# Optimization experiments

Measured on AMD Instinct MI355X. Metric: run time of the kernel, lower is better.

Reference implementation:

```python
import jax, jax.numpy as jnp
import numpy as np

DIM = 1024
N_HEAD = 16
HEAD_DIM = DIM // N_HEAD
B, T = 2, 2048


def setup_inputs() -> dict:
    key = jax.random.key(0)
    ks = jax.random.split(key, 9)
    s = 1.0 / np.sqrt(DIM)
    return {
        "x": jax.random.normal(ks[0], (B, T, DIM), dtype=jnp.float32),
        "Wq": jax.random.normal(ks[1], (DIM, DIM), dtype=jnp.float32) * s,
        "bq": jax.random.normal(ks[2], (DIM,), dtype=jnp.float32) * s,
        "Wk": jax.random.normal(ks[3], (DIM, DIM), dtype=jnp.float32) * s,
        "bk": jax.random.normal(ks[4], (DIM,), dtype=jnp.float32) * s,
        "Wv": jax.random.normal(ks[5], (DIM, DIM), dtype=jnp.float32) * s,
        "bv": jax.random.normal(ks[6], (DIM,), dtype=jnp.float32) * s,
        "Wo": jax.random.normal(ks[7], (DIM, DIM), dtype=jnp.float32) * s,
        "bo": jax.random.normal(ks[8], (DIM,), dtype=jnp.float32) * s,
    }


def reference(x, Wq, bq, Wk, bk, Wv, bv, Wo, bo):
    b, t, d = x.shape
    # torch nn.Linear: y = x @ W.T + b
    Q = x @ Wq.T + bq  # [b, t, d]
    K = x @ Wk.T + bk
    V = x @ Wv.T + bv
    # split heads -> [b, h, t, hd]
    Q = Q.reshape(b, t, N_HEAD, HEAD_DIM).transpose(0, 2, 1, 3)
    K = K.reshape(b, t, N_HEAD, HEAD_DIM).transpose(0, 2, 1, 3)
    V = V.reshape(b, t, N_HEAD, HEAD_DIM).transpose(0, 2, 1, 3)
    scale = 1.0 / jnp.sqrt(jnp.float32(HEAD_DIM))
    score = jnp.einsum('bhqd,bhkd->bhqk', Q, K) * scale  # [b, h, t, t]
    attn = jax.nn.softmax(score, axis=-1)
    # dropout is identity in eval mode
    out = jnp.einsum('bhqk,bhkd->bhqd', attn, V)  # [b, h, t, hd]
    out = out.transpose(0, 2, 1, 3).reshape(b, t, d)
    return out @ Wo.T + bo
```

## Files before the change

### kernel.cpp

```cpp
#include <hip/hip_runtime.h>


#define DIM 1024
#define NH 16
#define HD 64
#define SEQ 2048
#define NROWS 4096

typedef unsigned short u16;
typedef unsigned int u32;
typedef __bf16 bf16_t;
typedef bf16_t bf16x8 __attribute__((ext_vector_type(8)));
typedef float f32x4 __attribute__((ext_vector_type(4)));
typedef u16 u16x4 __attribute__((ext_vector_type(4)));
typedef short i16x4 __attribute__((ext_vector_type(4)));
typedef u32 u32x2 __attribute__((ext_vector_type(2)));

typedef const __attribute__((address_space(1))) void* gas_ptr;
typedef __attribute__((address_space(3))) void* las_ptr;

#define S_BARRIER() asm volatile("s_barrier" ::: "memory")
#define S_WAITCNT_VM(N) asm volatile("s_waitcnt vmcnt(" #N ")" ::: "memory")

__device__ __forceinline__ void gl_lds16(const void* g, void* lds_wave_base) {
  __builtin_amdgcn_global_load_lds((gas_ptr)g, (las_ptr)lds_wave_base, 16, 0, 0);
}

__device__ __forceinline__ f32x4 mfma_bf16(bf16x8 a, bf16x8 b, f32x4 c) {
  return __builtin_amdgcn_mfma_f32_16x16x32_bf16(a, b, c, 0, 0, 0);
}

__device__ __forceinline__ f32x4 mfma16_bf16(i16x4 a, i16x4 b, f32x4 c) {
#if __has_builtin(__builtin_amdgcn_mfma_f32_16x16x16bf16_1k)
  return __builtin_amdgcn_mfma_f32_16x16x16bf16_1k(a, b, c, 0, 0, 0);
#else
  asm("v_mfma_f32_16x16x16_bf16 %0, %1, %2, %0" : "+v"(c) : "v"(a), "v"(b));
  return c;
#endif
}

__device__ __forceinline__ u32 cvtpk(float lo, float hi) {
  u32 r;
  asm("v_cvt_pk_bf16_f32 %0, %1, %2" : "=v"(r) : "v"(lo), "v"(hi));
  return r;
}

__device__ __forceinline__ u16 bfu(float f) {
  bf16_t b = (bf16_t)f;
  union { bf16_t b; u16 u; } cv; cv.b = b; return cv.u;
}

__device__ __forceinline__ float fexp2(float x) {
#if __has_builtin(__builtin_amdgcn_exp2f)
  return __builtin_amdgcn_exp2f(x);
#else
  return exp2f(x);
#endif
}

#define QSCALE 0.18033688f

__global__ void cvt_x(const float* __restrict__ in, u16* __restrict__ out) {
  int i = blockIdx.x * 256 + threadIdx.x;
  float4 v = ((const float4*)in)[i];
  u16x4 o;
  o.x = bfu(v.x); o.y = bfu(v.y); o.z = bfu(v.z); o.w = bfu(v.w);
  ((u16x4*)out)[i] = o;
}

__global__ void cvt_w4(const float* __restrict__ wq, const float* __restrict__ wk,
                       const float* __restrict__ wv, const float* __restrict__ wo,
                       u16* __restrict__ oq, u16* __restrict__ ok,
                       u16* __restrict__ ov, u16* __restrict__ oo) {
  const int which = blockIdx.y;
  const float* in = which == 0 ? wq : which == 1 ? wk : which == 2 ? wv : wo;
  u16* out = which == 0 ? oq : which == 1 ? ok : which == 2 ? ov : oo;
  const float s = which == 0 ? QSCALE : 1.0f;
  int i = blockIdx.x * 256 + threadIdx.x;
  float4 v = ((const float4*)in)[i];
  u16x4 o;
  o.x = bfu(v.x * s); o.y = bfu(v.y * s); o.z = bfu(v.z * s); o.w = bfu(v.w * s);
  ((u16x4*)out)[i] = o;
}

__device__ __forceinline__ int xcd_swz(int L, int nwg) {
  return (L & 7) * (nwg >> 3) + (L >> 3);
}

__global__ __launch_bounds__(256, 3) void gemm_qkv(const u16* __restrict__ A,
                                                   const u16* __restrict__ wq,
                                                   const u16* __restrict__ wk,
                                                   const u16* __restrict__ wv,
                                                   const float* __restrict__ bq,
                                                   const float* __restrict__ bk,
                                                   const float* __restrict__ bv,
                                                   u16* __restrict__ Qb,
                                                   u16* __restrict__ Kb,
                                                   u16* __restrict__ Vtb) {
  __shared__ u16 As[2][128 * 32];
  __shared__ u16 Bs[2][128 * 32];
  const int L = blockIdx.y * gridDim.x + blockIdx.x;
  const int swz = xcd_swz(L, gridDim.x * gridDim.y);
  const int bx = swz % gridDim.x, by = swz / gridDim.x;
  const int which = bx >> 3;
  const int col0 = (bx & 7) * 128;
  const u16* W = which == 0 ? wq : which == 1 ? wk : wv;
  const float* bias = which == 0 ? bq : which == 1 ? bk : bv;
  const float bscale = which == 0 ? QSCALE : 1.0f;

  const int t = threadIdx.x, lane = t & 63, w = t >> 6;
  const int row0 = by * 128;
  const int wr = w >> 1, wc = w & 1;
  const int lr = lane & 15, lk = lane >> 4;

  f32x4 acc[4][4] = {};

  auto stage = [&](int k0, int bu) {
#pragma unroll
    for (int i = 0; i < 2; ++i) {
      const int bc = i * 256 + w * 64;
      const int f = bc + lane;
      gl_lds16(A + (size_t)(row0 + (f >> 2)) * DIM + k0 + (f & 3) * 8, &As[bu][bc * 8]);
      gl_lds16(W + (size_t)(col0 + (f >> 2)) * DIM + k0 + (f & 3) * 8, &Bs[bu][bc * 8]);
    }
  };

  stage(0, 0);
  int buf = 0;
  for (int k0 = 0; k0 < DIM; k0 += 32) {
    if (k0 + 32 < DIM) { stage(k0 + 32, buf ^ 1); S_WAITCNT_VM(4); }
    else               { S_WAITCNT_VM(0); }
    S_BARRIER();

    bf16x8 a[4], b[4];
#pragma unroll
    for (int m = 0; m < 4; ++m)
      a[m] = *(const bf16x8*)&As[buf][(wr * 64 + m * 16 + lr) * 32 + lk * 8];
#pragma unroll
    for (int n = 0; n < 4; ++n)
      b[n] = *(const bf16x8*)&Bs[buf][(wc * 64 + n * 16 + lr) * 32 + lk * 8];
    __builtin_amdgcn_s_setprio(1);
#pragma unroll
    for (int m = 0; m < 4; ++m)
#pragma unroll
      for (int n = 0; n < 4; ++n)
        acc[m][n] = mfma_bf16(a[m], b[n], acc[m][n]);
    __builtin_amdgcn_s_setprio(0);

    S_BARRIER();
    buf ^= 1;
  }

#pragma unroll
  for (int m = 0; m < 4; ++m) {
    const int rowb = row0 + wr * 64 + m * 16 + lk * 4;
#pragma unroll
    for (int n = 0; n < 4; ++n) {
      const int ocol = col0 + wc * 64 + n * 16 + lr;
      const float bc = bias[ocol] * bscale;
#pragma unroll
      for (int r = 0; r < 4; ++r) {
        const int rr = rowb + r;
        const float v = acc[m][n][r] + bc;
        if (which == 0) {
          Qb[(size_t)rr * DIM + ocol] = bfu(v);
        } else if (which == 1) {
          Kb[(size_t)rr * DIM + ocol] = bfu(v);
        } else {
          const size_t idx = ((((size_t)(rr >> 11) * NH + (ocol >> 6)) * HD + (ocol & 63)) << 11) + (rr & 2047);
          Vtb[idx] = bfu(v);
        }
      }
    }
  }
}

__global__ __launch_bounds__(256, 3) void gemm_out(const u16* __restrict__ A,
                                                   const u16* __restrict__ W,
                                                   const float* __restrict__ bias,
                                                   float* __restrict__ C) {
  __shared__ u16 As[2][128 * 32];
  __shared__ u16 Bs[2][128 * 32];
  const int L = blockIdx.y * gridDim.x + blockIdx.x;
  const int swz = xcd_swz(L, gridDim.x * gridDim.y);
  const int bx = swz % gridDim.x, by = swz / gridDim.x;
  const int t = threadIdx.x, lane = t & 63, w = t >> 6;
  const int row0 = by * 128, col0 = bx * 128;
  const int wr = w >> 1, wc = w & 1;
  const int lr = lane & 15, lk = lane >> 4;

  f32x4 acc[4][4] = {};

  auto stage = [&](int k0, int bu) {
#pragma unroll
    for (int i = 0; i < 2; ++i) {
      const int bc = i * 256 + w * 64;
      const int f = bc + lane;
      gl_lds16(A + (size_t)(row0 + (f >> 2)) * DIM + k0 + (f & 3) * 8, &As[bu][bc * 8]);
      gl_lds16(W + (size_t)(col0 + (f >> 2)) * DIM + k0 + (f & 3) * 8, &Bs[bu][bc * 8]);
    }
  };

  stage(0, 0);
  int buf = 0;
  for (int k0 = 0; k0 < DIM; k0 += 32) {
    if (k0 + 32 < DIM) { stage(k0 + 32, buf ^ 1); S_WAITCNT_VM(4); }
    else               { S_WAITCNT_VM(0); }
    S_BARRIER();

    bf16x8 a[4], b[4];
#pragma unroll
    for (int m = 0; m < 4; ++m)
      a[m] = *(const bf16x8*)&As[buf][(wr * 64 + m * 16 + lr) * 32 + lk * 8];
#pragma unroll
    for (int n = 0; n < 4; ++n)
      b[n] = *(const bf16x8*)&Bs[buf][(wc * 64 + n * 16 + lr) * 32 + lk * 8];
    __builtin_amdgcn_s_setprio(1);
#pragma unroll
    for (int m = 0; m < 4; ++m)
#pragma unroll
      for (int n = 0; n < 4; ++n)
        acc[m][n] = mfma_bf16(a[m], b[n], acc[m][n]);
    __builtin_amdgcn_s_setprio(0);

    S_BARRIER();
    buf ^= 1;
  }

#pragma unroll
  for (int m = 0; m < 4; ++m) {
    const int rowb = row0 + wr * 64 + m * 16 + lk * 4;
#pragma unroll
    for (int n = 0; n < 4; ++n) {
      const int col = col0 + wc * 64 + n * 16 + lr;
      const float bc = bias[col];
#pragma unroll
      for (int r = 0; r < 4; ++r)
        C[(size_t)(rowb + r) * DIM + col] = acc[m][n][r] + bc;
    }
  }
}

__global__ __launch_bounds__(256, 5) void flash_attn(const u16* __restrict__ Q,
                                                     const u16* __restrict__ K,
                                                     const u16* __restrict__ Vt,
                                                     u16* __restrict__ O) {
  __shared__ u16 Ks[2][64 * 64];
  __shared__ u16 Vs[2][64 * 64];

  const int t = threadIdx.x, lane = t & 63, w = t >> 6;
  const int L = blockIdx.x;
  const int bh = ((L >> 8) << 3) | (L & 7);
  const int qt = (L >> 3) & 31;
  const int b = bh >> 4, h = bh & 15;
  const int q0 = qt * 64;
  const int lr = lane & 15, lk = lane >> 4;

  const size_t qrow = (size_t)(b * SEQ + q0 + w * 16 + lr);
  bf16x8 qf[2];
  qf[0] = *(const bf16x8*)&Q[qrow * DIM + h * HD + lk * 8];
  qf[1] = *(const bf16x8*)&Q[qrow * DIM + h * HD + lk * 8 + 32];

  f32x4 o[4] = {};
  float m0 = -INFINITY, l0 = 0.f;

  auto stage = [&](int kt, int bu) {
#pragma unroll
    for (int i = 0; i < 2; ++i) {
      const int bc = i * 256 + w * 64;
      const int f = bc + lane;
      const int row = f >> 3, c = f & 7;
      const int cs = c ^ (row & 7);
      gl_lds16(K + (size_t)(b * SEQ + kt + row) * DIM + h * HD + cs * 8, &Ks[bu][bc * 8]);
      gl_lds16(Vt + (((size_t)bh * HD + row) << 11) + kt + cs * 8, &Vs[bu][bc * 8]);
    }
  };

  stage(0, 0);
  int buf = 0;
  for (int kt = 0; kt < SEQ; kt += 64) {
    if (kt + 64 < SEQ) { stage(kt + 64, buf ^ 1); S_WAITCNT_VM(4); }
    else               { S_WAITCNT_VM(0); }
    S_BARRIER();

    const u16* ks = Ks[buf];
    const u16* vs = Vs[buf];

    f32x4 s[4] = {};
    __builtin_amdgcn_s_setprio(1);
#pragma unroll
    for (int n = 0; n < 4; ++n) {
      const int row = n * 16 + lr;
#pragma unroll
      for (int kk = 0; kk < 2; ++kk) {
        bf16x8 kf = *(const bf16x8*)&ks[row * 64 + (((lk + kk * 4) ^ (row & 7)) * 8)];
        s[n] = mfma_bf16(kf, qf[kk], s[n]);
      }
    }
    __builtin_amdgcn_s_setprio(0);

    f32x4 m4 = s[0];
#pragma unroll
    for (int n = 1; n < 4; ++n) {
      m4[0] = fmaxf(m4[0], s[n][0]); m4[1] = fmaxf(m4[1], s[n][1]);
      m4[2] = fmaxf(m4[2], s[n][2]); m4[3] = fmaxf(m4[3], s[n][3]);
    }
    float mx = fmaxf(fmaxf(m4[0], m4[1]), fmaxf(m4[2], m4[3]));
    mx = fmaxf(mx, __shfl_xor(mx, 16));
    mx = fmaxf(mx, __shfl_xor(mx, 32));
    if (__any(mx > m0 + 8.0f)) {
      const float mnew = fmaxf(m0, mx);
      const float alpha = fexp2(m0 - mnew);
      m0 = mnew;
      l0 *= alpha;
#pragma unroll
      for (int r = 0; r < 4; ++r) {
        const float a_r = __shfl(alpha, lk * 4 + r);
#pragma unroll
        for (int nd = 0; nd < 4; ++nd) o[nd][r] *= a_r;
      }
    }

    float p[4][4];
    float rs = 0.f;
#pragma unroll
    for (int n = 0; n < 4; ++n)
#pragma unroll
      for (int r = 0; r < 4; ++r) { p[n][r] = fexp2(s[n][r] - m0); rs += p[n][r]; }
    rs += __shfl_xor(rs, 16);
    rs += __shfl_xor(rs, 32);
    l0 += rs;

    i16x4 paf[4];
#pragma unroll
    for (int n = 0; n < 4; ++n) {
      u32x2 pk;
      pk[0] = cvtpk(p[n][0], p[n][1]);
      pk[1] = cvtpk(p[n][2], p[n][3]);
      paf[n] = __builtin_bit_cast(i16x4, pk);
    }

    __builtin_amdgcn_s_setprio(1);
#pragma unroll
    for (int n = 0; n < 4; ++n) {
#pragma unroll
      for (int nd = 0; nd < 4; ++nd) {
        const int vrow = nd * 16 + lr;
        const int chunk = (2 * n + (lk >> 1)) ^ (vrow & 7);
        i16x4 vb = *(const i16x4*)&vs[vrow * 64 + chunk * 8 + (lk & 1) * 4];
        o[nd] = mfma16_bf16(paf[n], vb, o[nd]);
      }
    }
    __builtin_amdgcn_s_setprio(0);

    S_BARRIER();
    buf ^= 1;
  }

#pragma unroll
  for (int r = 0; r < 4; ++r) {
    const float inv = 1.f / __shfl(l0, lk * 4 + r);
    const size_t grow = (size_t)(b * SEQ + q0 + w * 16 + lk * 4 + r);
#pragma unroll
    for (int nd = 0; nd < 4; ++nd)
      O[grow * DIM + h * HD + nd * 16 + lr] = bfu(o[nd][r] * inv);
  }
}

extern "C" void kernel_launch(void* const* d_in, const int* in_sizes, int n_in,
                              void* d_out, int out_size, void* d_ws, size_t ws_size,
                              hipStream_t stream) {
  (void)in_sizes; (void)n_in; (void)out_size; (void)ws_size;
  const float* x  = (const float*)d_in[0];
  const float* Wq = (const float*)d_in[1];
  const float* bq = (const float*)d_in[2];
  const float* Wk = (const float*)d_in[3];
  const float* bk = (const float*)d_in[4];
  const float* Wv = (const float*)d_in[5];
  const float* bv = (const float*)d_in[6];
  const float* Wo = (const float*)d_in[7];
  const float* bo = (const float*)d_in[8];

  char* ws = (char*)d_ws;
  u16* xb  = (u16*)(ws + 0);
  u16* wqb = (u16*)(ws + 8388608);
  u16* wkb = (u16*)(ws + 10485760);
  u16* wvb = (u16*)(ws + 12582912);
  u16* wob = (u16*)(ws + 14680064);
  u16* Qb  = (u16*)(ws + 16777216);
  u16* Kb  = (u16*)(ws + 25165824);
  u16* Vtb = (u16*)(ws + 33554432);
  u16* Ob  = (u16*)(ws + 41943040);

  cvt_x<<<NROWS * DIM / 4 / 256, 256, 0, stream>>>(x, xb);
  cvt_w4<<<dim3(DIM * DIM / 4 / 256, 4), 256, 0, stream>>>(Wq, Wk, Wv, Wo, wqb, wkb, wvb, wob);

  gemm_qkv<<<dim3(24, NROWS / 128), 256, 0, stream>>>(xb, wqb, wkb, wvb, bq, bk, bv, Qb, Kb, Vtb);

  flash_attn<<<1024, 256, 0, stream>>>(Qb, Kb, Vtb, Ob);

  gemm_out<<<dim3(DIM / 128, NROWS / 128), 256, 0, stream>>>(Ob, wob, bo, (float*)d_out);
}
```

Baseline: 139.5 us.

## Split attention over two KV halves with a combine kernel and LDS-staged P

Splits each query tile's key range into two halves processed by separate blocks, doubling the grid and raising occupancy (launch bounds 8). Each block writes unnormalized partial outputs plus running max and sum, and a new combine kernel merges them with log-sum-exp rescaling. The KV tile shrinks to 32, and probabilities are staged through LDS so PV uses the wider 16x16x32 MFMA. This adds an extra kernel launch and extra global traffic for the partial results.

```diff
diff --git a/kernel.cpp b/kernel.cpp
--- a/kernel.cpp
+++ b/kernel.cpp
@@ -13,7 +13,6 @@
 typedef bf16_t bf16x8 __attribute__((ext_vector_type(8)));
 typedef float f32x4 __attribute__((ext_vector_type(4)));
 typedef u16 u16x4 __attribute__((ext_vector_type(4)));
-typedef short i16x4 __attribute__((ext_vector_type(4)));
 typedef u32 u32x2 __attribute__((ext_vector_type(2)));
 
 typedef const __attribute__((address_space(1))) void* gas_ptr;
@@ -28,15 +27,6 @@
 
 __device__ __forceinline__ f32x4 mfma_bf16(bf16x8 a, bf16x8 b, f32x4 c) {
   return __builtin_amdgcn_mfma_f32_16x16x32_bf16(a, b, c, 0, 0, 0);
-}
-
-__device__ __forceinline__ f32x4 mfma16_bf16(i16x4 a, i16x4 b, f32x4 c) {
-#if __has_builtin(__builtin_amdgcn_mfma_f32_16x16x16bf16_1k)
-  return __builtin_amdgcn_mfma_f32_16x16x16bf16_1k(a, b, c, 0, 0, 0);
-#else
-  asm("v_mfma_f32_16x16x16_bf16 %0, %1, %2, %0" : "+v"(c) : "v"(a), "v"(b));
-  return c;
-#endif
 }
 
 __device__ __forceinline__ u32 cvtpk(float lo, float hi) {
@@ -48,6 +38,10 @@
 __device__ __forceinline__ u16 bfu(float f) {
   bf16_t b = (bf16_t)f;
   union { bf16_t b; u16 u; } cv; cv.b = b; return cv.u;
+}
+
+__device__ __forceinline__ float b2f(u16 u) {
+  union { u32 u; float f; } cv; cv.u = ((u32)u) << 16; return cv.f;
 }
 
 __device__ __forceinline__ float fexp2(float x) {
@@ -241,17 +235,22 @@
   }
 }
 
-__global__ __launch_bounds__(256, 5) void flash_attn(const u16* __restrict__ Q,
-                                                     const u16* __restrict__ K,
-                                                     const u16* __restrict__ Vt,
-                                                     u16* __restrict__ O) {
-  __shared__ u16 Ks[2][64 * 64];
-  __shared__ u16 Vs[2][64 * 64];
+__global__ __launch_bounds__(256, 8) void flash_split(const u16* __restrict__ Q,
+                                                      const u16* __restrict__ K,
+                                                      const u16* __restrict__ Vt,
+                                                      u16* __restrict__ Op0,
+                                                      u16* __restrict__ Op1,
+                                                      float2* __restrict__ ml0,
+                                                      float2* __restrict__ ml1) {
+  __shared__ u16 Ks[2][32 * 64];
+  __shared__ u16 Vs[2][64 * 32];
+  __shared__ u16 Ps[4][16 * 32];
 
   const int t = threadIdx.x, lane = t & 63, w = t >> 6;
   const int L = blockIdx.x;
-  const int bh = ((L >> 8) << 3) | (L & 7);
-  const int qt = (L >> 3) & 31;
+  const int bh = ((L >> 9) << 3) | (L & 7);
+  const int inner = (L >> 3) & 63;
+  const int qt = inner >> 1, half = inner & 1;
   const int b = bh >> 4, h = bh & 15;
   const int q0 = qt * 64;
   const int lr = lane & 15, lk = lane >> 4;
@@ -264,47 +263,42 @@
   f32x4 o[4] = {};
   float m0 = -INFINITY, l0 = 0.f;
 
+  const int kbase = half * (SEQ / 2);
+
   auto stage = [&](int kt, int bu) {
-#pragma unroll
-    for (int i = 0; i < 2; ++i) {
-      const int bc = i * 256 + w * 64;
-      const int f = bc + lane;
-      const int row = f >> 3, c = f & 7;
-      const int cs = c ^ (row & 7);
-      gl_lds16(K + (size_t)(b * SEQ + kt + row) * DIM + h * HD + cs * 8, &Ks[bu][bc * 8]);
-      gl_lds16(Vt + (((size_t)bh * HD + row) << 11) + kt + cs * 8, &Vs[bu][bc * 8]);
-    }
+    const int f = w * 64 + lane;
+    const int krow = f >> 3, kc = (f & 7) ^ (krow & 7);
+    gl_lds16(K + (size_t)(b * SEQ + kt + krow) * DIM + h * HD + kc * 8, &Ks[bu][w * 512]);
+    const int vrow = f >> 2, vc = (f & 3) ^ (vrow & 3);
+    gl_lds16(Vt + (((size_t)bh * HD + vrow) << 11) + kt + vc * 8, &Vs[bu][w * 512]);
   };
 
-  stage(0, 0);
+  stage(kbase, 0);
   int buf = 0;
-  for (int kt = 0; kt < SEQ; kt += 64) {
-    if (kt + 64 < SEQ) { stage(kt + 64, buf ^ 1); S_WAITCNT_VM(4); }
-    else               { S_WAITCNT_VM(0); }
+  for (int kt = kbase; kt < kbase + SEQ / 2; kt += 32) {
+    if (kt + 32 < kbase + SEQ / 2) { stage(kt + 32, buf ^ 1); S_WAITCNT_VM(2); }
+    else                           { S_WAITCNT_VM(0); }
     S_BARRIER();
 
     const u16* ks = Ks[buf];
     const u16* vs = Vs[buf];
 
-    f32x4 s[4] = {};
+    f32x4 s[2] = {};
     __builtin_amdgcn_s_setprio(1);
 #pragma unroll
-    for (int n = 0; n < 4; ++n) {
+    for (int n = 0; n < 2; ++n) {
       const int row = n * 16 + lr;
 #pragma unroll
       for (int kk = 0; kk < 2; ++kk) {
-        bf16x8 kf = *(const bf16x8*)&ks[row * 64 + (((lk + kk * 4) ^ (row & 7)) * 8)];
+        bf16x8 kf = *(const bf16x8*)&ks[row * 64 + (((lk + kk * 4) ^ (lr & 7)) * 8)];
         s[n] = mfma_bf16(kf, qf[kk], s[n]);
       }
     }
     __builtin_amdgcn_s_setprio(0);
 
-    f32x4 m4 = s[0];
-#pragma unroll
-    for (int n = 1; n < 4; ++n) {
-      m4[0] = fmaxf(m4[0], s[n][0]); m4[1] = fmaxf(m4[1], s[n][1]);
-      m4[2] = fmaxf(m4[2], s[n][2]); m4[3] = fmaxf(m4[3], s[n][3]);
-    }
+    f32x4 m4;
+    m4[0] = fmaxf(s[0][0], s[1][0]); m4[1] = fmaxf(s[0][1], s[1][1]);
+    m4[2] = fmaxf(s[0][2], s[1][2]); m4[3] = fmaxf(s[0][3], s[1][3]);
     float mx = fmaxf(fmaxf(m4[0], m4[1]), fmaxf(m4[2], m4[3]));
     mx = fmaxf(mx, __shfl_xor(mx, 16));
     mx = fmaxf(mx, __shfl_xor(mx, 32));
@@ -321,35 +315,31 @@
       }
     }
 
-    float p[4][4];
+    float p[2][4];
     float rs = 0.f;
 #pragma unroll
-    for (int n = 0; n < 4; ++n)
+    for (int n = 0; n < 2; ++n)
 #pragma unroll
       for (int r = 0; r < 4; ++r) { p[n][r] = fexp2(s[n][r] - m0); rs += p[n][r]; }
     rs += __shfl_xor(rs, 16);
     rs += __shfl_xor(rs, 32);
     l0 += rs;
 
-    i16x4 paf[4];
-#pragma unroll
-    for (int n = 0; n < 4; ++n) {
-      u32x2 pk;
-      pk[0] = cvtpk(p[n][0], p[n][1]);
-      pk[1] = cvtpk(p[n][2], p[n][3]);
-      paf[n] = __builtin_bit_cast(i16x4, pk);
-    }
-
+#pragma unroll
+    for (int n = 0; n < 2; ++n) {
+      u32x2 d2;
+      d2[0] = cvtpk(p[n][0], p[n][1]);
+      d2[1] = cvtpk(p[n][2], p[n][3]);
+      *(u32x2*)&Ps[w][lr * 32 + (((n * 2 + (lk >> 1)) ^ (lr & 3)) * 8 + (lk & 1) * 4)] = d2;
+    }
+
+    bf16x8 pa = *(const bf16x8*)&Ps[w][lr * 32 + ((lk ^ (lr & 3)) * 8)];
     __builtin_amdgcn_s_setprio(1);
 #pragma unroll
-    for (int n = 0; n < 4; ++n) {
-#pragma unroll
-      for (int nd = 0; nd < 4; ++nd) {
-        const int vrow = nd * 16 + lr;
-        const int chunk = (2 * n + (lk >> 1)) ^ (vrow & 7);
-        i16x4 vb = *(const i16x4*)&vs[vrow * 64 + chunk * 8 + (lk & 1) * 4];
-        o[nd] = mfma16_bf16(paf[n], vb, o[nd]);
-      }
+    for (int nd = 0; nd < 4; ++nd) {
+      const int vrow = nd * 16 + lr;
+      bf16x8 vf = *(const bf16x8*)&vs[vrow * 32 + ((lk ^ (lr & 3)) * 8)];
+      o[nd] = mfma_bf16(pa, vf, o[nd]);
     }
     __builtin_amdgcn_s_setprio(0);
 
@@ -357,14 +347,47 @@
     buf ^= 1;
   }
 
+  u16* Op = half ? Op1 : Op0;
 #pragma unroll
   for (int r = 0; r < 4; ++r) {
-    const float inv = 1.f / __shfl(l0, lk * 4 + r);
-    const size_t grow = (size_t)(b * SEQ + q0 + w * 16 + lk * 4 + r);
+    const size_t prow = (size_t)bh * SEQ + q0 + w * 16 + lk * 4 + r;
 #pragma unroll
     for (int nd = 0; nd < 4; ++nd)
-      O[grow * DIM + h * HD + nd * 16 + lr] = bfu(o[nd][r] * inv);
-  }
+      Op[prow * HD + nd * 16 + lr] = bfu(o[nd][r]);
+  }
+  if (lk == 0) {
+    float2 v; v.x = m0; v.y = l0;
+    (half ? ml1 : ml0)[((size_t)bh << 11) + q0 + w * 16 + lr] = v;
+  }
+}
+
+__global__ __launch_bounds__(256) void combine(const u16* __restrict__ Op0,
+                                               const u16* __restrict__ Op1,
+                                               const float2* __restrict__ ml0,
+                                               const float2* __restrict__ ml1,
+                                               u16* __restrict__ Ob) {
+  const int t = threadIdx.x;
+  const int bh = blockIdx.y;
+  const int q = blockIdx.x * 16 + (t >> 4);
+  const int d0 = (t & 15) * 4;
+  const int b = bh >> 4, hh = bh & 15;
+
+  const float2 a0 = ml0[((size_t)bh << 11) + q];
+  const float2 a1 = ml1[((size_t)bh << 11) + q];
+  const float M = fmaxf(a0.x, a1.x);
+  float e0 = fexp2(a0.x - M);
+  float e1 = fexp2(a1.x - M);
+  const float inv = 1.f / (e0 * a0.y + e1 * a1.y);
+  e0 *= inv; e1 *= inv;
+
+  const size_t base = (((size_t)bh << 11) + q) * HD + d0;
+  const u16x4 v0 = *(const u16x4*)&Op0[base];
+  const u16x4 v1 = *(const u16x4*)&Op1[base];
+  u16x4 ov;
+#pragma unroll
+  for (int j = 0; j < 4; ++j)
+    ov[j] = bfu(e0 * b2f(v0[j]) + e1 * b2f(v1[j]));
+  *(u16x4*)&Ob[(size_t)(b * SEQ + q) * DIM + hh * HD + d0] = ov;
 }
 
 extern "C" void kernel_launch(void* const* d_in, const int* in_sizes, int n_in,
@@ -391,13 +414,18 @@
   u16* Kb  = (u16*)(ws + 25165824);
   u16* Vtb = (u16*)(ws + 33554432);
   u16* Ob  = (u16*)(ws + 41943040);
+  u16*    Op0 = (u16*)(ws + 0);
+  float2* ml0 = (float2*)(ws + 8388608);
+  float2* ml1 = (float2*)(ws + 8912896);
+  u16*    Op1 = (u16*)(ws + 50331648);
 
   cvt_x<<<NROWS * DIM / 4 / 256, 256, 0, stream>>>(x, xb);
   cvt_w4<<<dim3(DIM * DIM / 4 / 256, 4), 256, 0, stream>>>(Wq, Wk, Wv, Wo, wqb, wkb, wvb, wob);
 
   gemm_qkv<<<dim3(24, NROWS / 128), 256, 0, stream>>>(xb, wqb, wkb, wvb, bq, bk, bv, Qb, Kb, Vtb);
 
-  flash_attn<<<1024, 256, 0, stream>>>(Qb, Kb, Vtb, Ob);
+  flash_split<<<2048, 256, 0, stream>>>(Qb, Kb, Vtb, Op0, Op1, ml0, ml1);
+  combine<<<dim3(SEQ / 16, 2 * NH), 256, 0, stream>>>(Op0, Op1, ml0, ml1, Ob);
 
   gemm_out<<<dim3(DIM / 128, NROWS / 128), 256, 0, stream>>>(Ob, wob, bo, (float*)d_out);
 }
```

New measurement: 156.2 us. +11.9%, slower.
